# Kernel tuning notes

Measured on AMD Instinct MI355X. Metric: run time of the kernel, lower is better.

The kernel has to match this reference:

```python
import jax, jax.numpy as jnp
import numpy as np
from jax import lax

VOCAB = 10000
HID = 512
BATCH = 128
SEQ = 64
SCALE = 0.1


def setup_inputs() -> dict:
    key = jax.random.key(0)
    ks = jax.random.split(key, 16)
    u = lambda k, shape: jax.random.uniform(k, shape, jnp.float32, -SCALE, SCALE)
    return {
        "features": jax.random.randint(ks[0], (BATCH, SEQ), 0, VOCAB, jnp.int32),
        "labels": jax.random.randint(ks[1], (BATCH, SEQ), 0, VOCAB, jnp.int32),
        "seq_lengths": jax.random.randint(ks[2], (BATCH,), 0, SEQ, jnp.int32),
        "seq_mask": jax.random.uniform(ks[3], (BATCH, SEQ), jnp.float32),
        "embedding": u(ks[4], (VOCAB, HID)),
        "W0x": u(ks[5], (HID, 4 * HID)),
        "W0h": u(ks[6], (HID, 4 * HID)),
        "b0": jnp.zeros((4 * HID,), jnp.float32),
        "W1x": u(ks[7], (HID, 4 * HID)),
        "W1h": u(ks[8], (HID, 4 * HID)),
        "b1": jnp.zeros((4 * HID,), jnp.float32),
        "softmax_w": u(ks[9], (HID, VOCAB)),
        "softmax_b": jnp.zeros((VOCAB,), jnp.float32),
    }


def _lstm_cell(h, c, xin, Wx, Wh, b, m):
    # forget_bias = 0.0 (as in LSTMBlockCell(forget_bias=0.0))
    g = xin @ Wx + h @ Wh + b            # [B, 4H]
    i, cg, f, o = jnp.split(g, 4, axis=-1)
    c_new = jax.nn.sigmoid(f) * c + jax.nn.sigmoid(i) * jnp.tanh(cg)
    h_new = jax.nn.sigmoid(o) * jnp.tanh(c_new)
    # sequence_length masking: freeze state, zero output past length
    return m * h_new + (1 - m) * h, m * c_new + (1 - m) * c, m * h_new


def reference(features, labels, seq_lengths, seq_mask, embedding,
              W0x, W0h, b0, W1x, W1h, b1, softmax_w, softmax_b):
    x = embedding[features]                       # [B, T, H]
    B, T, H = x.shape
    xs = jnp.swapaxes(x, 0, 1)                    # [T, B, H]
    act = (jnp.arange(T)[:, None] < seq_lengths[None, :]).astype(x.dtype)[..., None]  # [T,B,1]

    def step(carry, inp):
        h0, c0, h1, c1 = carry
        xt, m = inp
        h0, c0, o0 = _lstm_cell(h0, c0, xt, W0x, W0h, b0, m)
        h1, c1, o1 = _lstm_cell(h1, c1, o0, W1x, W1h, b1, m)
        return (h0, c0, h1, c1), o1

    init = tuple(jnp.zeros((B, H), x.dtype) for _ in range(4))
    _, outs = lax.scan(step, init, (xs, act))     # [T, B, H]
    out = jnp.swapaxes(outs, 0, 1)                # [B, T, H]

    logits = out @ softmax_w + softmax_b          # [B, T, V]
    logp = jax.nn.log_softmax(logits, axis=-1)
    xent = -jnp.take_along_axis(logp, labels[..., None], axis=-1)[..., 0]  # [B, T]
    # tf.contrib.seq2seq.sequence_loss(average_across_batch=True, average_across_timesteps=False)
    loss_t = jnp.sum(xent * seq_mask, axis=0) / (jnp.sum(seq_mask, axis=0) + 1e-12)  # [T]
    cost = jnp.mean(loss_t)
    return cost
```

## Files before the change

kernel.cpp:

```cpp
#include <hip/hip_runtime.h>
#include <hip/hip_bf16.h>

#define BB 128
#define TT 64
#define HH 512
#define VV 10000
#define VP 10048
#define NTILES 157
#define NCHUNK 16
#define TPC 10
#define NBLK 256

typedef __attribute__((ext_vector_type(8))) __bf16 bf16x8;
typedef __attribute__((ext_vector_type(4))) float f32x4;
typedef unsigned short ushort_t;

__device__ __forceinline__ ushort_t f2bf(float x) {
  union { float f; unsigned u; } v; v.f = x;
  unsigned r = v.u + 0x7fffu + ((v.u >> 16) & 1u);
  return (ushort_t)(r >> 16);
}

__device__ __forceinline__ f32x4 mfma16(bf16x8 a, bf16x8 b, f32x4 c) {
  return __builtin_amdgcn_mfma_f32_16x16x32_bf16(a, b, c, 0, 0, 0);
}

__device__ __forceinline__ float fsig(float x) {
  return __builtin_amdgcn_rcpf(1.f + __expf(-x));
}
__device__ __forceinline__ float ftanh(float x) {
  return 1.f - 2.f * __builtin_amdgcn_rcpf(__expf(2.f * x) + 1.f);
}

__device__ __forceinline__ bf16x8 load16_sc1(const ushort_t* p) {
  bf16x8 r;
  asm volatile("global_load_dwordx4 %0, %1, off sc1" : "=v"(r) : "v"(p) : "memory");
  return r;
}

__device__ __forceinline__ void store16B_sc1(ushort_t* p, bf16x8 v) {
  asm volatile("global_store_dwordx4 %0, %1, off sc1" :: "v"(p), "v"(v) : "memory");
}

__device__ __forceinline__ void glds16(const ushort_t* g, ushort_t* l) {
  __builtin_amdgcn_global_load_lds(
      (const __attribute__((address_space(1))) unsigned*)g,
      (__attribute__((address_space(3))) unsigned*)l, 16, 0, 0);
}

__global__ __launch_bounds__(256) void k_prep(
    const float* __restrict__ Wx0, const float* __restrict__ Wh0,
    const float* __restrict__ Wx1, const float* __restrict__ Wh1,
    ushort_t* __restrict__ dst0, ushort_t* __restrict__ dst1,
    const float* __restrict__ sw, ushort_t* __restrict__ swt,
    const int* __restrict__ feat, const float* __restrict__ emb,
    ushort_t* __restrict__ xb, ushort_t* __restrict__ h0,
    ushort_t* __restrict__ h1, unsigned* __restrict__ bar) {
  __shared__ float tile[64][65];
  const int bid = blockIdx.x;
  const int tid = threadIdx.x;

  if (bid < 1024) {
    const int kt = (bid & 15) * 64;
    const int col0 = ((bid >> 4) & 31) * 64;
    const int z = bid >> 9;
    const float* Wx = z ? Wx1 : Wx0;
    const float* Wh = z ? Wh1 : Wh0;
    ushort_t* dst = z ? dst1 : dst0;
    const int cl = tid & 63;
    const int col = col0 + cl;
#pragma unroll
    for (int r = 0; r < 16; ++r) {
      const int kl = r * 4 + (tid >> 6);
      const int k = kt + kl;
      tile[kl][cl] = (k < 512) ? Wx[k * 2048 + col] : Wh[(k - 512) * 2048 + col];
    }
    __syncthreads();
#pragma unroll
    for (int s = 0; s < 16; ++s) {
      const int idx = tid + s * 256;
      const int cl2 = idx >> 6, kl2 = idx & 63;
      const int col2 = col0 + cl2;
      const int cp = ((col2 & 511) << 2) | (col2 >> 9);
      dst[(size_t)cp * 1024 + kt + kl2] = f2bf(tile[kl2][cl2]);
    }
  } else if (bid < 2280) {
    const int b = bid - 1024;
    const int kt = (b & 7) * 64;
    const int vt = (b >> 3) * 64;
    const int vl = tid & 63;
    const int v = vt + vl;
#pragma unroll
    for (int r = 0; r < 16; ++r) {
      const int kl = r * 4 + (tid >> 6);
      tile[vl][kl] = (v < VV) ? sw[(size_t)(kt + kl) * VV + v] : 0.f;
    }
    __syncthreads();
#pragma unroll
    for (int s = 0; s < 16; ++s) {
      const int idx = tid + s * 256;
      const int vl2 = idx >> 6, kl2 = idx & 63;
      const int k = kt + kl2;
      const int kb = k >> 3;
      const int kp = (((kb ^ (vl2 & 7)) << 3) | (k & 7));
      swt[(size_t)(vt + vl2) * 512 + kp] = f2bf(tile[vl2][kl2]);
    }
  } else {
    const int b = bid - 2280;
    for (int e = b * 256 + tid; e < 8192 * 512; e += 1024 * 256) {
      const int row = e >> 9;
      const int t = row >> 7, bb = row & 127;
      const int f = feat[bb * 64 + t];
      xb[e] = f2bf(emb[(size_t)f * 512 + (e & 511)]);
      if (e < 2 * 128 * 512) { h0[e] = 0; h1[e] = 0; }
      if (e < 1024) bar[e] = 0u;
    }
  }
}

__global__ __launch_bounds__(256, 1) void k_scan(
    const ushort_t* __restrict__ xb, const ushort_t* __restrict__ W0t,
    const ushort_t* __restrict__ W1t, const float* __restrict__ b0,
    const float* __restrict__ b1, ushort_t* __restrict__ h0g,
    ushort_t* __restrict__ h1g, ushort_t* __restrict__ out1,
    const int* __restrict__ seqlen, unsigned* __restrict__ bar) {
  __shared__ ushort_t act[32 * 128 * 8];
  __shared__ ushort_t hst[32][16];
  __shared__ ushort_t ost[32][16];
  __shared__ int sl_sh[32];
  const int bid = blockIdx.x;
  const int layer = bid >> 7;
  const int lb = bid & 127;
  const int cblk = lb >> 2;
  const int bquad = lb & 3;
  const int grp = bid & 3;
  const int tid = threadIdx.x;
  const int w = tid >> 6;
  const int lane = tid & 63;
  const int fr = lane & 15;
  const int hi = lane >> 4;
  const int w4hi = w * 4 + hi;

  const ushort_t* Wt = layer ? W1t : W0t;
  const float* bias = layer ? b1 : b0;
  ushort_t* hbuf = layer ? h1g : h0g;

  if (tid < 32) sl_sh[tid] = seqlen[bquad * 32 + tid];

  bf16x8 wreg[32];
  {
    const ushort_t* wp = Wt + (size_t)(cblk * 64 + w * 16 + fr) * 1024 + hi * 8;
#pragma unroll
    for (int ks = 0; ks < 32; ++ks)
      wreg[ks] = *reinterpret_cast<const bf16x8*>(wp + ks * 32);
  }

  const int u = cblk * 16 + w4hi;
  const float bi = bias[u];
  const float bc = bias[512 + u];
  const float bf_ = bias[1024 + u];
  const float bo = bias[1536 + u];

  __syncthreads();
  const int sl0 = sl_sh[fr];
  const int sl1 = sl_sh[fr + 16];

  float c0s = 0.f, c1s = 0.f;
  float h0s = 0.f, h1s = 0.f;

#pragma unroll 1
  for (int p = 0; p <= 64; ++p) {
    const int t = layer ? (p - 1) : p;
    const bool active = layer ? (p >= 1) : (p < 64);
    const unsigned target = (unsigned)(p + 1);

    f32x4 acc0 = (f32x4){0.f, 0.f, 0.f, 0.f};
    f32x4 acc1 = (f32x4){0.f, 0.f, 0.f, 0.f};

    asm volatile("s_waitcnt vmcnt(0)" ::: "memory");
    __syncthreads();
    if (tid == 0) {
      const unsigned old = __hip_atomic_fetch_add(&bar[grp * 16], 1u,
                                                  __ATOMIC_RELAXED, __HIP_MEMORY_SCOPE_AGENT);
      if (old + 1 == 64u * target)
        __hip_atomic_store(&bar[256 + grp * 16], target, __ATOMIC_RELAXED,
                           __HIP_MEMORY_SCOPE_AGENT);
    }
    if (layer == 0 && active) {
      const ushort_t* xsrc = xb + (size_t)t * 128 * 512;
#pragma unroll
      for (int i = 0; i < 8; ++i) {
        const int idx = i * 256 + tid;
        const int b = idx >> 6;
        const int kp = idx & 63;
        const int kslot = (kp & 0x30) | ((kp & 15) ^ (b & 15));
        const ushort_t* s = xsrc + (size_t)(bquad * 32 + b) * 512 + (kslot << 3);
        *reinterpret_cast<bf16x8*>(&act[(b * 128 + kp) * 8]) =
            *reinterpret_cast<const bf16x8*>(s);
      }
      __syncthreads();
#pragma unroll
      for (int ks = 0; ks < 16; ++ks) {
        const int kslot = ks * 4 + hi;
        const int kp = (kslot & 0x70) | ((kslot & 15) ^ fr);
        const bf16x8 bf0 = *reinterpret_cast<const bf16x8*>(&act[(fr * 128 + kp) * 8]);
        const bf16x8 bf1 = *reinterpret_cast<const bf16x8*>(&act[((16 + fr) * 128 + kp) * 8]);
        acc0 = mfma16(wreg[ks], bf0, acc0);
        acc1 = mfma16(wreg[ks], bf1, acc1);
      }
    }
    if (tid == 0) {
      while (__hip_atomic_load(&bar[256 + grp * 16], __ATOMIC_RELAXED,
                               __HIP_MEMORY_SCOPE_AGENT) < target)
        __builtin_amdgcn_s_sleep(1);
    }
    __syncthreads();

    if (active) {
      if (layer == 1) {
        bf16x8 tmp[16];
        const ushort_t* xsrc = h0g + (size_t)(p & 1) * 128 * 512;
        const ushort_t* hsrc = h1g + (size_t)(t & 1) * 128 * 512;
        int dsts[16];
#pragma unroll
        for (int i = 0; i < 8; ++i) {
          const int idx = i * 256 + tid;
          const int b = idx >> 6;
          const int kp = idx & 63;
          const int kslot = (kp & 0x30) | ((kp & 15) ^ (b & 15));
          tmp[i] = load16_sc1(xsrc + (size_t)(bquad * 32 + b) * 512 + (kslot << 3));
          dsts[i] = (b * 128 + kp) * 8;
        }
#pragma unroll
        for (int i = 0; i < 8; ++i) {
          const int idx = i * 256 + tid;
          const int b = idx >> 6;
          const int kp = 64 + (idx & 63);
          const int kslot = (kp & 0x70) | ((kp & 15) ^ (b & 15));
          tmp[8 + i] = load16_sc1(hsrc + (size_t)(bquad * 32 + b) * 512 + ((kslot - 64) << 3));
          dsts[8 + i] = (b * 128 + kp) * 8;
        }
        asm volatile("s_waitcnt vmcnt(0)" ::: "memory");
        __builtin_amdgcn_sched_barrier(0);
        const bf16x8 ZV = {};
#pragma unroll
        for (int i = 0; i < 8; ++i) {
          const int b = (i * 256 + tid) >> 6;
          *reinterpret_cast<bf16x8*>(&act[dsts[i]]) = (t < sl_sh[b]) ? tmp[i] : ZV;
        }
#pragma unroll
        for (int i = 0; i < 8; ++i)
          *reinterpret_cast<bf16x8*>(&act[dsts[8 + i]]) = tmp[8 + i];
        __syncthreads();
#pragma unroll
        for (int ks = 0; ks < 32; ++ks) {
          const int kslot = ks * 4 + hi;
          const int kp = (kslot & 0x70) | ((kslot & 15) ^ fr);
          const bf16x8 bf0 = *reinterpret_cast<const bf16x8*>(&act[(fr * 128 + kp) * 8]);
          const bf16x8 bf1 = *reinterpret_cast<const bf16x8*>(&act[((16 + fr) * 128 + kp) * 8]);
          acc0 = mfma16(wreg[ks], bf0, acc0);
          acc1 = mfma16(wreg[ks], bf1, acc1);
        }
      } else {
        bf16x8 tmp[8];
        const ushort_t* hsrc = h0g + (size_t)(t & 1) * 128 * 512;
        int dsts[8];
#pragma unroll
        for (int i = 0; i < 8; ++i) {
          const int idx = i * 256 + tid;
          const int b = idx >> 6;
          const int kp = 64 + (idx & 63);
          const int kslot = (kp & 0x70) | ((kp & 15) ^ (b & 15));
          tmp[i] = load16_sc1(hsrc + (size_t)(bquad * 32 + b) * 512 + ((kslot - 64) << 3));
          dsts[i] = (b * 128 + kp) * 8;
        }
        asm volatile("s_waitcnt vmcnt(0)" ::: "memory");
        __builtin_amdgcn_sched_barrier(0);
#pragma unroll
        for (int i = 0; i < 8; ++i)
          *reinterpret_cast<bf16x8*>(&act[dsts[i]]) = tmp[i];
        __syncthreads();
#pragma unroll
        for (int ks = 16; ks < 32; ++ks) {
          const int kslot = ks * 4 + hi;
          const int kp = (kslot & 0x70) | ((kslot & 15) ^ fr);
          const bf16x8 bf0 = *reinterpret_cast<const bf16x8*>(&act[(fr * 128 + kp) * 8]);
          const bf16x8 bf1 = *reinterpret_cast<const bf16x8*>(&act[((16 + fr) * 128 + kp) * 8]);
          acc0 = mfma16(wreg[ks], bf0, acc0);
          acc1 = mfma16(wreg[ks], bf1, acc1);
        }
      }
      __syncthreads();

      {
        const float si = fsig(acc0[0] + bi);
        const float tc = ftanh(acc0[1] + bc);
        const float sf = fsig(acc0[2] + bf_);
        const float so = fsig(acc0[3] + bo);
        const float cn = sf * c0s + si * tc;
        const float hn = so * ftanh(cn);
        const bool msk = t < sl0;
        if (msk) { c0s = cn; h0s = hn; }
        hst[fr][w4hi] = f2bf(h0s);
        if (layer) ost[fr][w4hi] = msk ? f2bf(hn) : (ushort_t)0;
      }
      {
        const float si = fsig(acc1[0] + bi);
        const float tc = ftanh(acc1[1] + bc);
        const float sf = fsig(acc1[2] + bf_);
        const float so = fsig(acc1[3] + bo);
        const float cn = sf * c1s + si * tc;
        const float hn = so * ftanh(cn);
        const bool msk = t < sl1;
        if (msk) { c1s = cn; h1s = hn; }
        hst[fr + 16][w4hi] = f2bf(h1s);
        if (layer) ost[fr + 16][w4hi] = msk ? f2bf(hn) : (ushort_t)0;
      }
      __syncthreads();

      if (tid < 64) {
        const int bl = tid >> 1, hf = tid & 1;
        const size_t off = (size_t)(bquad * 32 + bl) * 512 + cblk * 16 + hf * 8;
        ushort_t* hp = hbuf + (size_t)((t + 1) & 1) * 128 * 512 + off;
        const bf16x8 hv = *reinterpret_cast<const bf16x8*>(&hst[bl][hf * 8]);
        store16B_sc1(hp, hv);
        if (layer) {
          const bf16x8 ovv = *reinterpret_cast<const bf16x8*>(&ost[bl][hf * 8]);
          *reinterpret_cast<bf16x8*>(out1 + (size_t)t * 128 * 512 + off) = ovv;
        }
      }
    }
  }
}

__global__ __launch_bounds__(256, 2) void k_loss_gemm(
    const ushort_t* __restrict__ A, const ushort_t* __restrict__ SWTs,
    const float* __restrict__ sb, const int* __restrict__ labels,
    float* __restrict__ part) {
  __shared__ ushort_t Bl[2][32 * 512];
  __shared__ float sbl[640];
  const int tid = threadIdx.x;
  const int lane = tid & 63;
  const int w = tid >> 6;
  const int fr = lane & 15;
  const int fk = (lane >> 4) << 3;
  const int chunk = blockIdx.x & 15;
  const int rowbase = (blockIdx.x >> 4) * 128 + w * 32;
  const int tile_lo = chunk * TPC;
  const int tile_hi = (tile_lo + TPC < NTILES) ? (tile_lo + TPC) : NTILES;
  const int nhalf = (tile_hi - tile_lo) * 2;

  for (int i = tid; i < 640; i += 256) {
    const int v = chunk * 640 + i;
    sbl[i] = (v < VV) ? sb[v] : 0.f;
  }

  bf16x8 a[2][16];
#pragma unroll
  for (int rf = 0; rf < 2; ++rf) {
    const ushort_t* ap = A + (size_t)(rowbase + rf * 16 + fr) * 512 + fk;
#pragma unroll
    for (int ks = 0; ks < 16; ++ks) a[rf][ks] = *reinterpret_cast<const bf16x8*>(ap + ks * 32);
  }

  int lab[2][4];
  float m[2][4], l[2][4], ll[2][4];
#pragma unroll
  for (int rf = 0; rf < 2; ++rf)
#pragma unroll
    for (int r = 0; r < 4; ++r) {
      const int rg = rowbase + rf * 16 + ((lane >> 4) << 2) + r;
      lab[rf][r] = labels[(rg & 127) * 64 + (rg >> 7)];
      m[rf][r] = -3.0e38f; l[rf][r] = 0.f; ll[rf][r] = 0.f;
    }
  __syncthreads();

#define STAGE(BUF, HIDX)                                                         \
  do {                                                                           \
    const size_t gbase = (size_t)(tile_lo * 2 + (HIDX)) * 32 * 512;              \
    _Pragma("unroll")                                                            \
    for (int i_ = 0; i_ < 8; ++i_) {                                             \
      glds16(SWTs + gbase + (size_t)(i_ * 256 + tid) * 8,                        \
             &Bl[BUF][i_ * 2048 + w * 512]);                                     \
    }                                                                            \
  } while (0)

  f32x4 acc[2][4];
  STAGE(0, 0);

#pragma unroll 1
  for (int idx = 0; idx < nhalf; ++idx) {
    const int cur = idx & 1;
    if (idx + 1 < nhalf) {
      STAGE(cur ^ 1, idx + 1);
      asm volatile("s_waitcnt vmcnt(8)" ::: "memory");
    } else {
      asm volatile("s_waitcnt vmcnt(0)" ::: "memory");
    }
    __builtin_amdgcn_s_barrier();
    __builtin_amdgcn_sched_barrier(0);

    if ((idx & 1) == 0) {
      acc[0][0] = (f32x4){0.f,0.f,0.f,0.f}; acc[0][1] = (f32x4){0.f,0.f,0.f,0.f};
      acc[1][0] = (f32x4){0.f,0.f,0.f,0.f}; acc[1][1] = (f32x4){0.f,0.f,0.f,0.f};
#pragma unroll
      for (int ks = 0; ks < 16; ++ks) {
#pragma unroll
        for (int j = 0; j < 2; ++j) {
          const int vloc = j * 16 + fr;
          const int kb = ks * 4 + (fk >> 3);
          const bf16x8 b = *reinterpret_cast<const bf16x8*>(
              &Bl[cur][vloc * 512 + ((kb ^ (vloc & 7)) << 3)]);
          acc[0][j] = mfma16(a[0][ks], b, acc[0][j]);
          acc[1][j] = mfma16(a[1][ks], b, acc[1][j]);
        }
      }
    } else {
      acc[0][2] = (f32x4){0.f,0.f,0.f,0.f}; acc[0][3] = (f32x4){0.f,0.f,0.f,0.f};
      acc[1][2] = (f32x4){0.f,0.f,0.f,0.f}; acc[1][3] = (f32x4){0.f,0.f,0.f,0.f};
#pragma unroll
      for (int ks = 0; ks < 16; ++ks) {
#pragma unroll
        for (int j = 0; j < 2; ++j) {
          const int vloc = j * 16 + fr;
          const int kb = ks * 4 + (fk >> 3);
          const bf16x8 b = *reinterpret_cast<const bf16x8*>(
              &Bl[cur][vloc * 512 + ((kb ^ (vloc & 7)) << 3)]);
          acc[0][2 + j] = mfma16(a[0][ks], b, acc[0][2 + j]);
          acc[1][2 + j] = mfma16(a[1][ks], b, acc[1][2 + j]);
        }
      }

      const int tl = idx >> 1;
      const int vb = (tile_lo + tl) * 64;
      float sbt[4]; bool vld[4];
#pragma unroll
      for (int cf = 0; cf < 4; ++cf) {
        const int v = vb + cf * 16 + fr;
        vld[cf] = v < VV;
        sbt[cf] = sbl[tl * 64 + cf * 16 + fr];
      }
#pragma unroll
      for (int rf = 0; rf < 2; ++rf)
#pragma unroll
        for (int r = 0; r < 4; ++r) {
          const float x0 = vld[0] ? acc[rf][0][r] + sbt[0] : -3.0e38f;
          const float x1 = vld[1] ? acc[rf][1][r] + sbt[1] : -3.0e38f;
          const float x2 = vld[2] ? acc[rf][2][r] + sbt[2] : -3.0e38f;
          const float x3 = vld[3] ? acc[rf][3][r] + sbt[3] : -3.0e38f;
          const float tm = fmaxf(fmaxf(x0, x1), fmaxf(x2, x3));
          if (tm > -1.0e37f) {
            const float mn = fmaxf(m[rf][r], tm);
            const float sc = __expf(m[rf][r] - mn);
            const float se = __expf(x0 - mn) + __expf(x1 - mn) +
                             __expf(x2 - mn) + __expf(x3 - mn);
            l[rf][r] = l[rf][r] * sc + se;
            m[rf][r] = mn;
          }
          const int lt = lab[rf][r] - vb;
          if (lt >= 0 && lt < 64 && fr == (lt & 15)) {
            const int cf = lt >> 4;
            ll[rf][r] += (cf == 0) ? x0 : (cf == 1) ? x1 : (cf == 2) ? x2 : x3;
          }
        }
    }
    __builtin_amdgcn_s_barrier();
  }
#undef STAGE

#pragma unroll
  for (int rf = 0; rf < 2; ++rf)
#pragma unroll
    for (int r = 0; r < 4; ++r) {
      float mm = m[rf][r], lv = l[rf][r], lv2 = ll[rf][r];
#pragma unroll
      for (int sh = 1; sh < 16; sh <<= 1) {
        const float m2 = __shfl_xor(mm, sh, 64);
        const float l2 = __shfl_xor(lv, sh, 64);
        const float ll2 = __shfl_xor(lv2, sh, 64);
        const float mn = fmaxf(mm, m2);
        lv = lv * __expf(mm - mn) + l2 * __expf(m2 - mn);
        mm = mn;
        lv2 += ll2;
      }
      if (fr == 0) {
        const int rg = rowbase + rf * 16 + ((lane >> 4) << 2) + r;
        float* p = part + ((size_t)chunk * 8192 + rg) * 4;
        p[0] = mm; p[1] = lv; p[2] = lv2;
      }
    }
}

__global__ void k_loss_merge(const float* __restrict__ part, float* __restrict__ xent) {
  const int row = blockIdx.x * 256 + threadIdx.x;
  float m = -3.0e38f, l = 0.f, ll = 0.f;
#pragma unroll
  for (int c = 0; c < NCHUNK; ++c) {
    const float* p = part + ((size_t)c * 8192 + row) * 4;
    const float pm = p[0], pl = p[1], pll = p[2];
    const float mn = fmaxf(m, pm);
    l = l * __expf(m - mn) + pl * __expf(pm - mn);
    m = mn;
    ll += pll;
  }
  xent[row] = m + logf(l) - ll;
}

__global__ void k_final(const float* __restrict__ xent, const float* __restrict__ mask,
                        float* __restrict__ out) {
  __shared__ float partial[4];
  const int lane = threadIdx.x & 63;
  const int w = threadIdx.x >> 6;
  float accT = 0.f;
  for (int i = 0; i < 16; ++i) {
    const int t = w * 16 + i;
    const float m1 = mask[lane * 64 + t];
    const float m2 = mask[(lane + 64) * 64 + t];
    float s = xent[t * 128 + lane] * m1 + xent[t * 128 + lane + 64] * m2;
    float sm = m1 + m2;
#pragma unroll
    for (int sh = 1; sh < 64; sh <<= 1) {
      s += __shfl_xor(s, sh, 64);
      sm += __shfl_xor(sm, sh, 64);
    }
    accT += s / (sm + 1e-12f);
  }
  if (lane == 0) partial[w] = accT;
  __syncthreads();
  if (threadIdx.x == 0)
    out[0] = (partial[0] + partial[1] + partial[2] + partial[3]) * (1.f / 64.f);
}

extern "C" void kernel_launch(void* const* d_in, const int* in_sizes, int n_in,
                              void* d_out, int out_size, void* d_ws, size_t ws_size,
                              hipStream_t stream) {
  const int* feat = (const int*)d_in[0];
  const int* labels = (const int*)d_in[1];
  const int* seqlen = (const int*)d_in[2];
  const float* seqmask = (const float*)d_in[3];
  const float* emb = (const float*)d_in[4];
  const float* W0x = (const float*)d_in[5];
  const float* W0h = (const float*)d_in[6];
  const float* b0 = (const float*)d_in[7];
  const float* W1x = (const float*)d_in[8];
  const float* W1h = (const float*)d_in[9];
  const float* b1 = (const float*)d_in[10];
  const float* sw = (const float*)d_in[11];
  const float* sbv = (const float*)d_in[12];

  ushort_t* W0t = (ushort_t*)d_ws;
  ushort_t* W1t = W0t + (size_t)2048 * 1024;
  ushort_t* SWT = W1t + (size_t)2048 * 1024;
  ushort_t* xb = SWT + (size_t)VP * 512;
  ushort_t* out1 = xb + (size_t)8192 * 512;
  ushort_t* h0g = out1 + (size_t)8192 * 512;
  ushort_t* h1g = h0g + (size_t)2 * 128 * 512;
  float* xent = (float*)(h1g + (size_t)2 * 128 * 512);
  float* part = xent + 8192;
  unsigned* bar = (unsigned*)(part + (size_t)NCHUNK * 8192 * 4);

  k_prep<<<dim3(3304), 256, 0, stream>>>(W0x, W0h, W1x, W1h, W0t, W1t,
                                         sw, SWT, feat, emb, xb, h0g, h1g, bar);

  {
    const ushort_t* a0 = xb; const ushort_t* a1 = W0t; const ushort_t* a2 = W1t;
    const float* a3 = b0; const float* a4 = b1;
    ushort_t* a5 = h0g; ushort_t* a6 = h1g; ushort_t* a7 = out1;
    const int* a8 = seqlen; unsigned* a9 = bar;
    void* args[] = {(void*)&a0, (void*)&a1, (void*)&a2, (void*)&a3, (void*)&a4,
                    (void*)&a5, (void*)&a6, (void*)&a7, (void*)&a8, (void*)&a9};
    hipLaunchCooperativeKernel((const void*)k_scan, dim3(NBLK), dim3(256), args, 0, stream);
  }

  k_loss_gemm<<<dim3(1024), 256, 0, stream>>>(out1, SWT, sbv, labels, part);
  k_loss_merge<<<32, 256, 0, stream>>>(part, xent);
  k_final<<<1, 256, 0, stream>>>(xent, seqmask, (float*)d_out);
}
```

Before: 461.6 us.

## Fuse LSTM scan and softmax-loss GEMM into one persistent kernel with worker blocks

Merges the recurrent scan and the vocabulary loss GEMM into one cooperative mega-kernel. 256 extra worker blocks poll the scan's per-group barrier flags and start computing logits and log-sum-exp partials for each timestep as soon as layer-1 output for that step is written. The aim is to hide the loss GEMM behind the latency-bound recurrence instead of running it afterward. The risks are that worker blocks compete with scan blocks for CUs and memory bandwidth, and that the cooperative launch of 512 blocks may fail, in which case the code falls back to the separate path.

Measured after the change: 814.0 us. 1.76x slower.

```diff
diff --git a/kernel.cpp b/kernel.cpp
--- a/kernel.cpp
+++ b/kernel.cpp
@@ -10,6 +10,7 @@
 #define NCHUNK 16
 #define TPC 10
 #define NBLK 256
+#define NWRK 256
 
 typedef __attribute__((ext_vector_type(8))) __bf16 bf16x8;
 typedef __attribute__((ext_vector_type(4))) float f32x4;
@@ -37,9 +38,13 @@
   asm volatile("global_load_dwordx4 %0, %1, off sc1" : "=v"(r) : "v"(p) : "memory");
   return r;
 }
-
 __device__ __forceinline__ void store16B_sc1(ushort_t* p, bf16x8 v) {
   asm volatile("global_store_dwordx4 %0, %1, off sc1" :: "v"(p), "v"(v) : "memory");
+}
+__device__ __forceinline__ unsigned load_flag_sc1(const unsigned* p) {
+  unsigned r;
+  asm volatile("global_load_dword %0, %1, off sc1" : "=v"(r) : "v"(p) : "memory");
+  return r;
 }
 
 __device__ __forceinline__ void glds16(const ushort_t* g, ushort_t* l) {
@@ -47,6 +52,18 @@
       (const __attribute__((address_space(1))) unsigned*)g,
       (__attribute__((address_space(3))) unsigned*)l, 16, 0, 0);
 }
+
+struct ScanSmem {
+  ushort_t act[32 * 128 * 8];
+  ushort_t hst[32][16];
+  ushort_t ost[32][16];
+  int sl_sh[32];
+};
+struct WorkSmem {
+  ushort_t Bl[2][32 * 512];
+  float sbl[640];
+};
+union MegaSmem { ScanSmem s; WorkSmem w; };
 
 __global__ __launch_bounds__(256) void k_prep(
     const float* __restrict__ Wx0, const float* __restrict__ Wh0,
@@ -118,17 +135,13 @@
   }
 }
 
-__global__ __launch_bounds__(256, 1) void k_scan(
+__device__ void scan_role(
+    ScanSmem* sm, int bid,
     const ushort_t* __restrict__ xb, const ushort_t* __restrict__ W0t,
     const ushort_t* __restrict__ W1t, const float* __restrict__ b0,
     const float* __restrict__ b1, ushort_t* __restrict__ h0g,
     ushort_t* __restrict__ h1g, ushort_t* __restrict__ out1,
     const int* __restrict__ seqlen, unsigned* __restrict__ bar) {
-  __shared__ ushort_t act[32 * 128 * 8];
-  __shared__ ushort_t hst[32][16];
-  __shared__ ushort_t ost[32][16];
-  __shared__ int sl_sh[32];
-  const int bid = blockIdx.x;
   const int layer = bid >> 7;
   const int lb = bid & 127;
   const int cblk = lb >> 2;
@@ -145,7 +158,7 @@
   const float* bias = layer ? b1 : b0;
   ushort_t* hbuf = layer ? h1g : h0g;
 
-  if (tid < 32) sl_sh[tid] = seqlen[bquad * 32 + tid];
+  if (tid < 32) sm->sl_sh[tid] = seqlen[bquad * 32 + tid];
 
   bf16x8 wreg[32];
   {
@@ -162,8 +175,8 @@
   const float bo = bias[1536 + u];
 
   __syncthreads();
-  const int sl0 = sl_sh[fr];
-  const int sl1 = sl_sh[fr + 16];
+  const int sl0 = sm->sl_sh[fr];
+  const int sl1 = sm->sl_sh[fr + 16];
 
   float c0s = 0.f, c1s = 0.f;
   float h0s = 0.f, h1s = 0.f;
@@ -195,7 +208,7 @@
         const int kp = idx & 63;
         const int kslot = (kp & 0x30) | ((kp & 15) ^ (b & 15));
         const ushort_t* s = xsrc + (size_t)(bquad * 32 + b) * 512 + (kslot << 3);
-        *reinterpret_cast<bf16x8*>(&act[(b * 128 + kp) * 8]) =
+        *reinterpret_cast<bf16x8*>(&sm->act[(b * 128 + kp) * 8]) =
             *reinterpret_cast<const bf16x8*>(s);
       }
       __syncthreads();
@@ -203,8 +216,8 @@
       for (int ks = 0; ks < 16; ++ks) {
         const int kslot = ks * 4 + hi;
         const int kp = (kslot & 0x70) | ((kslot & 15) ^ fr);
-        const bf16x8 bf0 = *reinterpret_cast<const bf16x8*>(&act[(fr * 128 + kp) * 8]);
-        const bf16x8 bf1 = *reinterpret_cast<const bf16x8*>(&act[((16 + fr) * 128 + kp) * 8]);
+        const bf16x8 bf0 = *reinterpret_cast<const bf16x8*>(&sm->act[(fr * 128 + kp) * 8]);
+        const bf16x8 bf1 = *reinterpret_cast<const bf16x8*>(&sm->act[((16 + fr) * 128 + kp) * 8]);
         acc0 = mfma16(wreg[ks], bf0, acc0);
         acc1 = mfma16(wreg[ks], bf1, acc1);
       }
@@ -246,18 +259,18 @@
 #pragma unroll
         for (int i = 0; i < 8; ++i) {
           const int b = (i * 256 + tid) >> 6;
-          *reinterpret_cast<bf16x8*>(&act[dsts[i]]) = (t < sl_sh[b]) ? tmp[i] : ZV;
+          *reinterpret_cast<bf16x8*>(&sm->act[dsts[i]]) = (t < sm->sl_sh[b]) ? tmp[i] : ZV;
         }
 #pragma unroll
         for (int i = 0; i < 8; ++i)
-          *reinterpret_cast<bf16x8*>(&act[dsts[8 + i]]) = tmp[8 + i];
+          *reinterpret_cast<bf16x8*>(&sm->act[dsts[8 + i]]) = tmp[8 + i];
         __syncthreads();
 #pragma unroll
         for (int ks = 0; ks < 32; ++ks) {
           const int kslot = ks * 4 + hi;
           const int kp = (kslot & 0x70) | ((kslot & 15) ^ fr);
-          const bf16x8 bf0 = *reinterpret_cast<const bf16x8*>(&act[(fr * 128 + kp) * 8]);
-          const bf16x8 bf1 = *reinterpret_cast<const bf16x8*>(&act[((16 + fr) * 128 + kp) * 8]);
+          const bf16x8 bf0 = *reinterpret_cast<const bf16x8*>(&sm->act[(fr * 128 + kp) * 8]);
+          const bf16x8 bf1 = *reinterpret_cast<const bf16x8*>(&sm->act[((16 + fr) * 128 + kp) * 8]);
           acc0 = mfma16(wreg[ks], bf0, acc0);
           acc1 = mfma16(wreg[ks], bf1, acc1);
         }
@@ -278,14 +291,14 @@
         __builtin_amdgcn_sched_barrier(0);
 #pragma unroll
         for (int i = 0; i < 8; ++i)
-          *reinterpret_cast<bf16x8*>(&act[dsts[i]]) = tmp[i];
+          *reinterpret_cast<bf16x8*>(&sm->act[dsts[i]]) = tmp[i];
         __syncthreads();
 #pragma unroll
         for (int ks = 16; ks < 32; ++ks) {
           const int kslot = ks * 4 + hi;
           const int kp = (kslot & 0x70) | ((kslot & 15) ^ fr);
-          const bf16x8 bf0 = *reinterpret_cast<const bf16x8*>(&act[(fr * 128 + kp) * 8]);
-          const bf16x8 bf1 = *reinterpret_cast<const bf16x8*>(&act[((16 + fr) * 128 + kp) * 8]);
+          const bf16x8 bf0 = *reinterpret_cast<const bf16x8*>(&sm->act[(fr * 128 + kp) * 8]);
+          const bf16x8 bf1 = *reinterpret_cast<const bf16x8*>(&sm->act[((16 + fr) * 128 + kp) * 8]);
           acc0 = mfma16(wreg[ks], bf0, acc0);
           acc1 = mfma16(wreg[ks], bf1, acc1);
         }
@@ -301,8 +314,8 @@
         const float hn = so * ftanh(cn);
         const bool msk = t < sl0;
         if (msk) { c0s = cn; h0s = hn; }
-        hst[fr][w4hi] = f2bf(h0s);
-        if (layer) ost[fr][w4hi] = msk ? f2bf(hn) : (ushort_t)0;
+        sm->hst[fr][w4hi] = f2bf(h0s);
+        if (layer) sm->ost[fr][w4hi] = msk ? f2bf(hn) : (ushort_t)0;
       }
       {
         const float si = fsig(acc1[0] + bi);
@@ -313,8 +326,8 @@
         const float hn = so * ftanh(cn);
         const bool msk = t < sl1;
         if (msk) { c1s = cn; h1s = hn; }
-        hst[fr + 16][w4hi] = f2bf(h1s);
-        if (layer) ost[fr + 16][w4hi] = msk ? f2bf(hn) : (ushort_t)0;
+        sm->hst[fr + 16][w4hi] = f2bf(h1s);
+        if (layer) sm->ost[fr + 16][w4hi] = msk ? f2bf(hn) : (ushort_t)0;
       }
       __syncthreads();
 
@@ -322,45 +335,50 @@
         const int bl = tid >> 1, hf = tid & 1;
         const size_t off = (size_t)(bquad * 32 + bl) * 512 + cblk * 16 + hf * 8;
         ushort_t* hp = hbuf + (size_t)((t + 1) & 1) * 128 * 512 + off;
-        const bf16x8 hv = *reinterpret_cast<const bf16x8*>(&hst[bl][hf * 8]);
+        const bf16x8 hv = *reinterpret_cast<const bf16x8*>(&sm->hst[bl][hf * 8]);
         store16B_sc1(hp, hv);
         if (layer) {
-          const bf16x8 ovv = *reinterpret_cast<const bf16x8*>(&ost[bl][hf * 8]);
-          *reinterpret_cast<bf16x8*>(out1 + (size_t)t * 128 * 512 + off) = ovv;
-        }
-      }
-    }
-  }
-}
-
-__global__ __launch_bounds__(256, 2) void k_loss_gemm(
+          const bf16x8 ovv = *reinterpret_cast<const bf16x8*>(&sm->ost[bl][hf * 8]);
+          store16B_sc1(out1 + (size_t)t * 128 * 512 + off, ovv);
+        }
+      }
+    }
+  }
+
+  asm volatile("s_waitcnt vmcnt(0)" ::: "memory");
+  __syncthreads();
+  if (tid == 0) {
+    const unsigned old = __hip_atomic_fetch_add(&bar[grp * 16], 1u,
+                                                __ATOMIC_RELAXED, __HIP_MEMORY_SCOPE_AGENT);
+    if (old + 1 == 64u * 66u)
+      __hip_atomic_store(&bar[256 + grp * 16], 66u, __ATOMIC_RELAXED,
+                         __HIP_MEMORY_SCOPE_AGENT);
+  }
+}
+
+template <bool SC1>
+__device__ void loss_job(
+    WorkSmem* sm, int t, int chunk,
     const ushort_t* __restrict__ A, const ushort_t* __restrict__ SWTs,
-    const float* __restrict__ sb, const int* __restrict__ labels,
-    float* __restrict__ part) {
-  __shared__ ushort_t Bl[2][32 * 512];
-  __shared__ float sbl[640];
+    const int* __restrict__ labels, float* __restrict__ part) {
   const int tid = threadIdx.x;
   const int lane = tid & 63;
   const int w = tid >> 6;
   const int fr = lane & 15;
   const int fk = (lane >> 4) << 3;
-  const int chunk = blockIdx.x & 15;
-  const int rowbase = (blockIdx.x >> 4) * 128 + w * 32;
+  const int rowbase = t * 128 + w * 32;
   const int tile_lo = chunk * TPC;
   const int tile_hi = (tile_lo + TPC < NTILES) ? (tile_lo + TPC) : NTILES;
   const int nhalf = (tile_hi - tile_lo) * 2;
 
-  for (int i = tid; i < 640; i += 256) {
-    const int v = chunk * 640 + i;
-    sbl[i] = (v < VV) ? sb[v] : 0.f;
-  }
-
   bf16x8 a[2][16];
 #pragma unroll
   for (int rf = 0; rf < 2; ++rf) {
     const ushort_t* ap = A + (size_t)(rowbase + rf * 16 + fr) * 512 + fk;
 #pragma unroll
-    for (int ks = 0; ks < 16; ++ks) a[rf][ks] = *reinterpret_cast<const bf16x8*>(ap + ks * 32);
+    for (int ks = 0; ks < 16; ++ks)
+      a[rf][ks] = SC1 ? load16_sc1(ap + ks * 32)
+                      : *reinterpret_cast<const bf16x8*>(ap + ks * 32);
   }
 
   int lab[2][4];
@@ -373,26 +391,28 @@
       lab[rf][r] = labels[(rg & 127) * 64 + (rg >> 7)];
       m[rf][r] = -3.0e38f; l[rf][r] = 0.f; ll[rf][r] = 0.f;
     }
+  asm volatile("s_waitcnt vmcnt(0)" ::: "memory");
+  __builtin_amdgcn_sched_barrier(0);
   __syncthreads();
 
-#define STAGE(BUF, HIDX)                                                         \
+#define WSTAGE(BUF, HIDX)                                                        \
   do {                                                                           \
     const size_t gbase = (size_t)(tile_lo * 2 + (HIDX)) * 32 * 512;              \
     _Pragma("unroll")                                                            \
     for (int i_ = 0; i_ < 8; ++i_) {                                             \
       glds16(SWTs + gbase + (size_t)(i_ * 256 + tid) * 8,                        \
-             &Bl[BUF][i_ * 2048 + w * 512]);                                     \
+             &sm->Bl[BUF][i_ * 2048 + w * 512]);                                 \
     }                                                                            \
   } while (0)
 
   f32x4 acc[2][4];
-  STAGE(0, 0);
+  WSTAGE(0, 0);
 
 #pragma unroll 1
   for (int idx = 0; idx < nhalf; ++idx) {
     const int cur = idx & 1;
     if (idx + 1 < nhalf) {
-      STAGE(cur ^ 1, idx + 1);
+      WSTAGE(cur ^ 1, idx + 1);
       asm volatile("s_waitcnt vmcnt(8)" ::: "memory");
     } else {
       asm volatile("s_waitcnt vmcnt(0)" ::: "memory");
@@ -410,7 +430,7 @@
           const int vloc = j * 16 + fr;
           const int kb = ks * 4 + (fk >> 3);
           const bf16x8 b = *reinterpret_cast<const bf16x8*>(
-              &Bl[cur][vloc * 512 + ((kb ^ (vloc & 7)) << 3)]);
+              &sm->Bl[cur][vloc * 512 + ((kb ^ (vloc & 7)) << 3)]);
           acc[0][j] = mfma16(a[0][ks], b, acc[0][j]);
           acc[1][j] = mfma16(a[1][ks], b, acc[1][j]);
         }
@@ -425,7 +445,7 @@
           const int vloc = j * 16 + fr;
           const int kb = ks * 4 + (fk >> 3);
           const bf16x8 b = *reinterpret_cast<const bf16x8*>(
-              &Bl[cur][vloc * 512 + ((kb ^ (vloc & 7)) << 3)]);
+              &sm->Bl[cur][vloc * 512 + ((kb ^ (vloc & 7)) << 3)]);
           acc[0][2 + j] = mfma16(a[0][ks], b, acc[0][2 + j]);
           acc[1][2 + j] = mfma16(a[1][ks], b, acc[1][2 + j]);
         }
@@ -438,7 +458,7 @@
       for (int cf = 0; cf < 4; ++cf) {
         const int v = vb + cf * 16 + fr;
         vld[cf] = v < VV;
-        sbt[cf] = sbl[tl * 64 + cf * 16 + fr];
+        sbt[cf] = sm->sbl[tl * 64 + cf * 16 + fr];
       }
 #pragma unroll
       for (int rf = 0; rf < 2; ++rf)
@@ -466,7 +486,7 @@
     }
     __builtin_amdgcn_s_barrier();
   }
-#undef STAGE
+#undef WSTAGE
 
 #pragma unroll
   for (int rf = 0; rf < 2; ++rf)
@@ -489,6 +509,71 @@
         p[0] = mm; p[1] = lv; p[2] = lv2;
       }
     }
+  __syncthreads();
+}
+
+__device__ void worker_role(
+    WorkSmem* sm, int wid,
+    const ushort_t* __restrict__ out1, const ushort_t* __restrict__ SWTs,
+    const float* __restrict__ sb, const int* __restrict__ labels,
+    float* __restrict__ part, const unsigned* __restrict__ bar) {
+  const int tid = threadIdx.x;
+  const int chunk = wid & 15;
+  for (int i = tid; i < 640; i += 256) {
+    const int v = chunk * 640 + i;
+    sm->sbl[i] = (v < VV) ? sb[v] : 0.f;
+  }
+
+#pragma unroll 1
+  for (int job_i = 0; job_i < 4; ++job_i) {
+    const int job = wid + job_i * NWRK;
+    const int t = job >> 4;
+
+    if (tid == 0) {
+      const unsigned need = (unsigned)(t + 3);
+      while (true) {
+        const unsigned g0 = load_flag_sc1(bar + 256 + 0);
+        const unsigned g1 = load_flag_sc1(bar + 256 + 16);
+        const unsigned g2 = load_flag_sc1(bar + 256 + 32);
+        const unsigned g3 = load_flag_sc1(bar + 256 + 48);
+        asm volatile("s_waitcnt vmcnt(0)" ::: "memory");
+        unsigned mn = g0 < g1 ? g0 : g1;
+        mn = mn < g2 ? mn : g2;
+        mn = mn < g3 ? mn : g3;
+        if (mn >= need) break;
+        __builtin_amdgcn_s_sleep(8);
+      }
+    }
+    __syncthreads();
+    loss_job<true>(sm, t, chunk, out1, SWTs, labels, part);
+  }
+}
+
+__global__ __launch_bounds__(256, 1) void k_mega(
+    const ushort_t* xb, const ushort_t* W0t, const ushort_t* W1t,
+    const float* b0, const float* b1, ushort_t* h0g, ushort_t* h1g,
+    ushort_t* out1, const int* seqlen, unsigned* bar,
+    const ushort_t* SWTs, const float* sb, const int* labels, float* part) {
+  __shared__ MegaSmem sm;
+  const int bid = blockIdx.x;
+  if (bid < NBLK)
+    scan_role(&sm.s, bid, xb, W0t, W1t, b0, b1, h0g, h1g, out1, seqlen, bar);
+  else
+    worker_role(&sm.w, bid - NBLK, out1, SWTs, sb, labels, part, bar);
+}
+
+__global__ __launch_bounds__(256, 2) void k_loss_std(
+    const ushort_t* __restrict__ A, const ushort_t* __restrict__ SWTs,
+    const float* __restrict__ sb, const int* __restrict__ labels,
+    float* __restrict__ part) {
+  __shared__ WorkSmem sm;
+  const int chunk = blockIdx.x & 15;
+  const int t = blockIdx.x >> 4;
+  for (int i = threadIdx.x; i < 640; i += 256) {
+    const int v = chunk * 640 + i;
+    sm.sbl[i] = (v < VV) ? sb[v] : 0.f;
+  }
+  loss_job<false>(&sm, t, chunk, A, SWTs, labels, part);
 }
 
 __global__ void k_loss_merge(const float* __restrict__ part, float* __restrict__ xent) {
@@ -562,17 +647,28 @@
   k_prep<<<dim3(3304), 256, 0, stream>>>(W0x, W0h, W1x, W1h, W0t, W1t,
                                          sw, SWT, feat, emb, xb, h0g, h1g, bar);
 
-  {
-    const ushort_t* a0 = xb; const ushort_t* a1 = W0t; const ushort_t* a2 = W1t;
-    const float* a3 = b0; const float* a4 = b1;
-    ushort_t* a5 = h0g; ushort_t* a6 = h1g; ushort_t* a7 = out1;
-    const int* a8 = seqlen; unsigned* a9 = bar;
-    void* args[] = {(void*)&a0, (void*)&a1, (void*)&a2, (void*)&a3, (void*)&a4,
-                    (void*)&a5, (void*)&a6, (void*)&a7, (void*)&a8, (void*)&a9};
-    hipLaunchCooperativeKernel((const void*)k_scan, dim3(NBLK), dim3(256), args, 0, stream);
-  }
-
-  k_loss_gemm<<<dim3(1024), 256, 0, stream>>>(out1, SWT, sbv, labels, part);
+  const ushort_t* a0 = xb; const ushort_t* a1 = W0t; const ushort_t* a2 = W1t;
+  const float* a3 = b0; const float* a4 = b1;
+  ushort_t* a5 = h0g; ushort_t* a6 = h1g; ushort_t* a7 = out1;
+  const int* a8 = seqlen; unsigned* a9 = bar;
+  const ushort_t* a10 = SWT; const float* a11 = sbv; const int* a12 = labels;
+  float* a13 = part;
+  void* args[] = {(void*)&a0, (void*)&a1, (void*)&a2, (void*)&a3, (void*)&a4,
+                  (void*)&a5, (void*)&a6, (void*)&a7, (void*)&a8, (void*)&a9,
+                  (void*)&a10, (void*)&a11, (void*)&a12, (void*)&a13};
+
+  hipError_t err = hipLaunchCooperativeKernel((const void*)k_mega,
+                                              dim3(NBLK + NWRK), dim3(256), args, 0, stream);
+  if (err != hipSuccess) {
+    hipError_t err2 = hipLaunchCooperativeKernel((const void*)k_mega,
+                                                 dim3(NBLK), dim3(256), args, 0, stream);
+    if (err2 != hipSuccess) {
+      k_mega<<<dim3(NBLK), 256, 0, stream>>>(xb, W0t, W1t, b0, b1, h0g, h1g,
+                                             out1, seqlen, bar, SWT, sbv, labels, part);
+    }
+    k_loss_std<<<dim3(1024), 256, 0, stream>>>(out1, SWT, sbv, labels, part);
+  }
+
   k_loss_merge<<<32, 256, 0, stream>>>(part, xent);
   k_final<<<1, 256, 0, stream>>>(xent, seqmask, (float*)d_out);
 }
```
